# Optimization experiments

Hardware: AMD Instinct MI355X
Metric: run time of the kernel (lower is better)

Reference implementation:

```python
import jax, jax.numpy as jnp
import numpy as np

N = 16384      # points
C = 512        # channels (d_model)
D_INNER = 1024 # expand=2
D_STATE = 16
D_CONV = 4
DT_RANK = 32   # ceil(C/16)
MLP = 1024     # mlp_ratio=2
EPS = 1e-5


def setup_inputs() -> dict:
    key = jax.random.key(0)
    ks = jax.random.split(key, 16)
    s = 0.02
    feat = jax.random.normal(ks[0], (N, C), jnp.float32)
    perm = np.random.RandomState(0).permutation(N)
    order = jnp.asarray(perm, jnp.int32)
    inverse = jnp.asarray(np.argsort(perm), jnp.int32)
    inp = dict(
        feat=feat, order=order, inverse=inverse,
        ln1_w=jnp.ones((C,)), ln1_b=jnp.zeros((C,)),
        in_proj_w=s * jax.random.normal(ks[1], (2 * D_INNER, C)),
        conv_w=s * jax.random.normal(ks[2], (D_INNER, D_CONV)),
        conv_b=jnp.zeros((D_INNER,)),
        x_proj_w=s * jax.random.normal(ks[3], (DT_RANK + 2 * D_STATE, D_INNER)),
        dt_proj_w=s * jax.random.normal(ks[4], (D_INNER, DT_RANK)),
        dt_proj_b=jnp.full((D_INNER,), -2.0),  # softplus(-2) ~ small dt, like mamba init
        A_log=jnp.log(jnp.tile(jnp.arange(1, D_STATE + 1, dtype=jnp.float32)[None, :], (D_INNER, 1))),
        D_skip=jnp.ones((D_INNER,)),
        out_proj_w=s * jax.random.normal(ks[5], (C, D_INNER)),
        ln2_w=jnp.ones((C,)), ln2_b=jnp.zeros((C,)),
        ffn_w1=s * jax.random.normal(ks[6], (C, MLP)), ffn_b1=jnp.zeros((MLP,)),
        ffn_w2=s * jax.random.normal(ks[7], (MLP, C)), ffn_b2=jnp.zeros((C,)),
    )
    return inp


def _layer_norm(x, w, b):
    mu = jnp.mean(x, axis=-1, keepdims=True)
    var = jnp.mean(jnp.square(x - mu), axis=-1, keepdims=True)
    return (x - mu) * jax.lax.rsqrt(var + EPS) * w + b


def _mamba(x, in_proj_w, conv_w, conv_b, x_proj_w, dt_proj_w, dt_proj_b,
           A_log, D_skip, out_proj_w):
    # x: (L, C)
    L = x.shape[0]
    xz = x @ in_proj_w.T                      # (L, 2*D_INNER)
    xm, z = jnp.split(xz, 2, axis=-1)
    # depthwise causal conv1d, kernel D_CONV
    xp = jnp.pad(xm, ((D_CONV - 1, 0), (0, 0)))
    xc = conv_b + sum(xp[k:k + L] * conv_w[:, k] for k in range(D_CONV))
    xc = jax.nn.silu(xc)                      # (L, D_INNER)
    dbc = xc @ x_proj_w.T                     # (L, DT_RANK + 2*D_STATE)
    dt, Bm, Cm = jnp.split(dbc, [DT_RANK, DT_RANK + D_STATE], axis=-1)
    dt = jax.nn.softplus(dt @ dt_proj_w.T + dt_proj_b)  # (L, D_INNER)
    A = -jnp.exp(A_log)                       # (D_INNER, D_STATE)

    def step(h, inp):
        dt_t, B_t, C_t, x_t = inp             # (D_INNER,), (D_STATE,), (D_STATE,), (D_INNER,)
        dA = jnp.exp(dt_t[:, None] * A)       # (D_INNER, D_STATE)
        h = dA * h + (dt_t * x_t)[:, None] * B_t[None, :]
        return h, h @ C_t                     # y_t: (D_INNER,)

    h0 = jnp.zeros((D_INNER, D_STATE), xm.dtype)
    _, ys = jax.lax.scan(step, h0, (dt, Bm, Cm, xc))
    y = (ys + xc * D_skip) * jax.nn.silu(z)
    return y @ out_proj_w.T                   # (L, C)


def reference(feat, order, inverse, ln1_w, ln1_b, in_proj_w, conv_w, conv_b,
              x_proj_w, dt_proj_w, dt_proj_b, A_log, D_skip, out_proj_w,
              ln2_w, ln2_b, ffn_w1, ffn_b1, ffn_w2, ffn_b2):
    f = feat[order]                           # gather by serialized order
    x = f + _mamba(_layer_norm(f, ln1_w, ln1_b), in_proj_w, conv_w, conv_b,
                   x_proj_w, dt_proj_w, dt_proj_b, A_log, D_skip, out_proj_w)
    h = _layer_norm(x, ln2_w, ln2_b)
    x = x + (jax.nn.gelu(h @ ffn_w1 + ffn_b1, approximate=False) @ ffn_w2 + ffn_b2)
    return x[inverse]                         # scatter back to original order
```

## Files before the change

kernel.cpp:

```cpp
#include <hip/hip_runtime.h>


#define DEV __device__ __forceinline__

typedef unsigned short u16;
typedef u16    u16x8  __attribute__((ext_vector_type(8)));
typedef __bf16 bf16x8 __attribute__((ext_vector_type(8)));
typedef float  f32x4  __attribute__((ext_vector_type(4)));

static constexpr int L_SEQ = 16384;
static constexpr int LC    = 64;
static constexpr int NCH   = 256;

DEV u16 f2b(float x){
  union { float f; unsigned u; } c; c.f = x;
  unsigned u = c.u;
  return (u16)((u + 0x7fffu + ((u >> 16) & 1u)) >> 16);
}
DEV float b2f(u16 h){
  union { unsigned u; float f; } c; c.u = ((unsigned)h) << 16;
  return c.f;
}
DEV int ldix(const void* p, int l, bool is64){
  return is64 ? (int)((const long long*)p)[l] : ((const int*)p)[l];
}
DEV float siluf(float x){ return x / (1.f + __expf(-x)); }
DEV float softplusf(float x){ return x > 20.f ? x : log1pf(__expf(x)); }
DEV float geluf(float x){ return 0.5f * x * (1.f + erff(x * 0.70710678118f)); }

DEV void gld_lds16(const u16* g, u16* l){
  __builtin_amdgcn_global_load_lds(
      (const __attribute__((address_space(1))) unsigned*)g,
      (__attribute__((address_space(3))) unsigned*)l, 16, 0, 0);
}

DEV void pow16(float r, float* a){
  float r2 = r * r, r4 = r2 * r2, r8 = r4 * r4;
  a[0] = r;        a[1] = r2;       a[2] = r2 * r;    a[3] = r4;
  a[4] = r4 * r;   a[5] = r4 * r2;  a[6] = r4 * a[2]; a[7] = r8;
  a[8] = r8 * r;   a[9] = r8 * r2;  a[10] = r8 * a[2]; a[11] = r8 * r4;
  a[12] = r8 * a[4]; a[13] = r8 * a[5]; a[14] = r8 * a[6]; a[15] = r8 * r8;
}

__global__ __launch_bounds__(256) void fill_k(float* out, float v, unsigned n){
  unsigned i = blockIdx.x * 256 + threadIdx.x;
  if (i < n) out[i] = v;
}

__global__ void detect_k(const int* ord32, int* flag){
  flag[0] = (ord32[1] == 0 && ord32[3] == 0 && ord32[5] == 0) ? 1 : 0;
  flag[1] = 0;
}

__global__ __launch_bounds__(256) void checkA_k(const float* __restrict__ alog,
                                                int* flag){
  int i = blockIdx.x * 256 + threadIdx.x;
  int s = i & 15;
  float v = alog[i];
  float base = alog[i - s];
  if (fabsf(v - (base + __logf((float)(s + 1)))) > 1e-4f) atomicOr(flag + 1, 1);
}

struct NT4 { const float* src[4]; unsigned off[5]; };
__global__ __launch_bounds__(256) void normw_k(NT4 t, u16* dst){
  unsigned i = blockIdx.x * 256 + threadIdx.x;
  if (i >= t.off[4]) return;
  int s = 0;
  #pragma unroll
  for (int k = 1; k <= 3; k++) s += (i >= t.off[k]) ? 1 : 0;
  dst[i] = f2b(t.src[s][i - t.off[s]]);
}

__global__ __launch_bounds__(256) void convT_kernel(const float* __restrict__ in,
                                                    u16* __restrict__ out, int K, int N){
  __shared__ float t[32][33];
  int k0 = blockIdx.x * 32, n0 = blockIdx.y * 32;
  int tx = threadIdx.x & 31, ty = threadIdx.x >> 5;
  #pragma unroll
  for (int i = 0; i < 32; i += 8)
    t[ty + i][tx] = in[(size_t)(k0 + ty + i) * N + n0 + tx];
  __syncthreads();
  #pragma unroll
  for (int i = 0; i < 32; i += 8)
    out[(size_t)(n0 + ty + i) * K + k0 + tx] = f2b(t[tx][ty + i]);
}

__global__ __launch_bounds__(256) void gather_ln1(const float* __restrict__ feat,
    const void* order, const float* __restrict__ w, const float* __restrict__ b,
    const int* flag, u16* __restrict__ x1b){
  __shared__ float rs_[256], rq_[256];
  const bool is64 = flag[0] != 0;
  int l = blockIdx.x, tid = threadIdx.x;
  int src = ldix(order, l, is64);
  float v0 = feat[(size_t)src * 512 + tid];
  float v1 = feat[(size_t)src * 512 + tid + 256];
  rs_[tid] = v0 + v1; rq_[tid] = v0 * v0 + v1 * v1;
  __syncthreads();
  for (int o = 128; o; o >>= 1){
    if (tid < o){ rs_[tid] += rs_[tid + o]; rq_[tid] += rq_[tid + o]; }
    __syncthreads();
  }
  float mu = rs_[0] * (1.f / 512.f);
  float var = rq_[0] * (1.f / 512.f) - mu * mu;
  float rstd = rsqrtf(var + 1e-5f);
  x1b[(size_t)l * 512 + tid]       = f2b((v0 - mu) * rstd * w[tid]       + b[tid]);
  x1b[(size_t)l * 512 + tid + 256] = f2b((v1 - mu) * rstd * w[tid + 256] + b[tid + 256]);
}

__global__ __launch_bounds__(256) void ln2_kernel(const float* __restrict__ x,
    const float* __restrict__ w, const float* __restrict__ b, u16* __restrict__ h2b){
  __shared__ float rs_[256], rq_[256];
  int l = blockIdx.x, tid = threadIdx.x;
  float v0 = x[(size_t)l * 512 + tid];
  float v1 = x[(size_t)l * 512 + tid + 256];
  rs_[tid] = v0 + v1; rq_[tid] = v0 * v0 + v1 * v1;
  __syncthreads();
  for (int o = 128; o; o >>= 1){
    if (tid < o){ rs_[tid] += rs_[tid + o]; rq_[tid] += rq_[tid + o]; }
    __syncthreads();
  }
  float mu = rs_[0] * (1.f / 512.f);
  float var = rq_[0] * (1.f / 512.f) - mu * mu;
  float rstd = rsqrtf(var + 1e-5f);
  h2b[(size_t)l * 512 + tid]       = f2b((v0 - mu) * rstd * w[tid]       + b[tid]);
  h2b[(size_t)l * 512 + tid + 256] = f2b((v1 - mu) * rstd * w[tid + 256] + b[tid + 256]);
}

__global__ __launch_bounds__(256) void conv_silu(const u16* __restrict__ xm,
    const float* __restrict__ cw, const float* __restrict__ cb, u16* __restrict__ xcb){
  constexpr int TT = 8;
  const int tid = threadIdx.x;
  const int d0 = (tid & 127) * 8;
  const int t0 = (blockIdx.x * 2 + (tid >> 7)) * TT;

  float wk[4][8], bias[8];
  #pragma unroll
  for (int j = 0; j < 8; j++) bias[j] = cb[d0 + j];
  #pragma unroll
  for (int j = 0; j < 8; j++){
    f32x4 v = *(const f32x4*)(cw + (d0 + j) * 4);
    wk[0][j] = v[0]; wk[1][j] = v[1]; wk[2][j] = v[2]; wk[3][j] = v[3];
  }

  float win[3][8];
  #pragma unroll
  for (int k = 0; k < 3; k++){
    int tt = t0 - 3 + k;
    if (tt >= 0){
      u16x8 v = *(const u16x8*)(xm + (size_t)tt * 1024 + d0);
      #pragma unroll
      for (int j = 0; j < 8; j++) win[k][j] = b2f(v[j]);
    } else {
      #pragma unroll
      for (int j = 0; j < 8; j++) win[k][j] = 0.f;
    }
  }

  #pragma unroll
  for (int t = 0; t < TT; t++){
    u16x8 v = *(const u16x8*)(xm + (size_t)(t0 + t) * 1024 + d0);
    u16x8 o;
    float cu[8];
    #pragma unroll
    for (int j = 0; j < 8; j++){
      cu[j] = b2f(v[j]);
      float acc = bias[j] + win[0][j] * wk[0][j] + win[1][j] * wk[1][j]
                + win[2][j] * wk[2][j] + cu[j] * wk[3][j];
      o[j] = f2b(siluf(acc));
    }
    *(u16x8*)(xcb + (size_t)(t0 + t) * 1024 + d0) = o;
    #pragma unroll
    for (int j = 0; j < 8; j++){
      win[0][j] = win[1][j]; win[1][j] = win[2][j]; win[2][j] = cu[j];
    }
  }
}

enum { M_BF16 = 0, M_INPROJ = 1, M_DT = 2, M_RES = 3, M_GELU = 4, M_FFN2 = 5 };

template<int MODE>
DEV void gemm_epilogue(float v, int m, int n, int N,
    float* __restrict__ outf, u16* __restrict__ outb, u16* __restrict__ outb2,
    const float* __restrict__ auxf, const float* __restrict__ auxw,
    const void* ordv, bool is64){
  size_t o = (size_t)m * N + n;
  if constexpr (MODE == M_BF16){
    outb[o] = f2b(v);
  } else if constexpr (MODE == M_INPROJ){
    if (n < 1024) outb [(size_t)m * 1024 + n]          = f2b(v);
    else          outb2[(size_t)m * 1024 + (n - 1024)] = f2b(siluf(v));
  } else if constexpr (MODE == M_DT){
    outb[o] = f2b(softplusf(v + auxw[n]));
  } else if constexpr (MODE == M_RES){
    int src = ldix(ordv, m, is64);
    outf[o] = v + auxw[(size_t)src * 512 + n];
  } else if constexpr (MODE == M_GELU){
    outb[o] = f2b(geluf(v + auxw[n]));
  } else {
    outf[o] = v + auxw[n] + auxf[o];
  }
}

template<int BM, int BN, int WM, int WN, int MODE>
__global__ __launch_bounds__(256) void gemm_bt64(
    const u16* __restrict__ A, const u16* __restrict__ B,
    int N, int K, int lda, int ldb,
    float* __restrict__ outf, u16* __restrict__ outb, u16* __restrict__ outb2,
    const float* __restrict__ auxf, const float* __restrict__ auxw,
    const void* ordv, const int* flag){
  constexpr int BK = 64;
  constexpr int MI = WM / 16, NI = WN / 16;
  constexpr int WCOLS = BN / WN;
  constexpr int NA = BM * BK / (256 * 8);
  constexpr int NB = BN * BK / (256 * 8);
  __shared__ __align__(16) u16 sA[2][BM * BK];
  __shared__ __align__(16) u16 sB[2][BN * BK];
  const int tid  = threadIdx.x;
  const int wave = tid >> 6, lane = tid & 63;
  const int wr = wave / WCOLS, wc = wave % WCOLS;
  const int m0 = blockIdx.x * BM, n0 = blockIdx.y * BN;
  const int rr = lane & 15;
  const int qh = lane >> 4;

  f32x4 acc[MI][NI] = {};

  auto stage = [&](int buf, int k0){
    #pragma unroll
    for (int i = 0; i < NA; i++){
      int idx = tid + i * 256;
      int row = idx >> 3, sub = idx & 7;
      int cg = sub ^ (row & 7);
      gld_lds16(A + (size_t)(m0 + row) * lda + k0 + cg * 8, &sA[buf][idx * 8]);
    }
    #pragma unroll
    for (int i = 0; i < NB; i++){
      int idx = tid + i * 256;
      int row = idx >> 3, sub = idx & 7;
      int cg = sub ^ (row & 7);
      gld_lds16(B + (size_t)(n0 + row) * ldb + k0 + cg * 8, &sB[buf][idx * 8]);
    }
  };

  stage(0, 0);
  const int nst = K / BK;
  for (int st = 0; st < nst; st++){
    const int cur = st & 1;
    __syncthreads();
    if (st + 1 < nst) stage(cur ^ 1, (st + 1) * BK);
    #pragma unroll
    for (int kk = 0; kk < 2; kk++){
      bf16x8 af[MI], bfr[NI];
      #pragma unroll
      for (int i = 0; i < MI; i++){
        int R = wr * WM + i * 16 + rr;
        int sub = (kk * 4 + qh) ^ (R & 7);
        af[i] = *(const bf16x8*)(&sA[cur][R * BK + sub * 8]);
      }
      #pragma unroll
      for (int j = 0; j < NI; j++){
        int R = wc * WN + j * 16 + rr;
        int sub = (kk * 4 + qh) ^ (R & 7);
        bfr[j] = *(const bf16x8*)(&sB[cur][R * BK + sub * 8]);
      }
      #pragma unroll
      for (int i = 0; i < MI; i++)
        #pragma unroll
        for (int j = 0; j < NI; j++)
          acc[i][j] = __builtin_amdgcn_mfma_f32_16x16x32_bf16(af[i], bfr[j], acc[i][j], 0, 0, 0);
    }
  }

  const bool is64 = flag ? (flag[0] != 0) : false;
  #pragma unroll
  for (int i = 0; i < MI; i++)
    #pragma unroll
    for (int j = 0; j < NI; j++)
      #pragma unroll
      for (int r = 0; r < 4; r++){
        int m = m0 + wr * WM + i * 16 + ((lane >> 4) << 2) + r;
        int n = n0 + wc * WN + j * 16 + (lane & 15);
        gemm_epilogue<MODE>(acc[i][j][r], m, n, N, outf, outb, outb2,
                            auxf, auxw, ordv, is64);
      }
}

template<int BM, int BN, int WM, int WN, int MODE>
__global__ __launch_bounds__(256) void gemm_bt(
    const u16* __restrict__ A, const u16* __restrict__ B,
    int N, int K, int lda, int ldb,
    float* __restrict__ outf, u16* __restrict__ outb, u16* __restrict__ outb2,
    const float* __restrict__ auxf, const float* __restrict__ auxw,
    const void* ordv, const int* flag){
  constexpr int BK = 32;
  constexpr int MI = WM / 16, NI = WN / 16;
  constexpr int WCOLS = BN / WN;
  constexpr int NA = BM * 4 / 256;
  constexpr int NB = BN * 4 / 256;
  __shared__ __align__(16) u16 sA[BM * BK];
  __shared__ __align__(16) u16 sB[BN * BK];
  const int tid  = threadIdx.x;
  const int wave = tid >> 6, lane = tid & 63;
  const int wr = wave / WCOLS, wc = wave % WCOLS;
  const int m0 = blockIdx.x * BM, n0 = blockIdx.y * BN;
  const int rr = lane & 15;
  const int qk = (lane >> 4) * 8;

  f32x4 acc[MI][NI] = {};

  for (int k0 = 0; k0 < K; k0 += BK){
    #pragma unroll
    for (int i = 0; i < NA; i++){
      int idx = tid + i * 256;
      int r = idx >> 2, c = (idx & 3) * 8;
      gld_lds16(A + (size_t)(m0 + r) * lda + k0 + c, sA + (size_t)idx * 8);
    }
    #pragma unroll
    for (int i = 0; i < NB; i++){
      int idx = tid + i * 256;
      int r = idx >> 2, c = (idx & 3) * 8;
      gld_lds16(B + (size_t)(n0 + r) * ldb + k0 + c, sB + (size_t)idx * 8);
    }
    __syncthreads();

    bf16x8 af[MI], bfr[NI];
    #pragma unroll
    for (int i = 0; i < MI; i++)
      af[i] = *(const bf16x8*)(sA + (wr * WM + i * 16 + rr) * BK + qk);
    #pragma unroll
    for (int j = 0; j < NI; j++)
      bfr[j] = *(const bf16x8*)(sB + (wc * WN + j * 16 + rr) * BK + qk);
    #pragma unroll
    for (int i = 0; i < MI; i++)
      #pragma unroll
      for (int j = 0; j < NI; j++)
        acc[i][j] = __builtin_amdgcn_mfma_f32_16x16x32_bf16(af[i], bfr[j], acc[i][j], 0, 0, 0);
    __syncthreads();
  }

  const bool is64 = flag ? (flag[0] != 0) : false;
  #pragma unroll
  for (int i = 0; i < MI; i++)
    #pragma unroll
    for (int j = 0; j < NI; j++)
      #pragma unroll
      for (int r = 0; r < 4; r++){
        int m = m0 + wr * WM + i * 16 + ((lane >> 4) << 2) + r;
        int n = n0 + wc * WN + j * 16 + (lane & 15);
        gemm_epilogue<MODE>(acc[i][j][r], m, n, N, outf, outb, outb2,
                            auxf, auxw, ordv, is64);
      }
}

__global__ __launch_bounds__(256) void scan_pass1(const u16* __restrict__ dt,
    const u16* __restrict__ xc, const u16* __restrict__ dbc,
    const float* __restrict__ alog, const int* __restrict__ flag,
    u16* __restrict__ chP, u16* __restrict__ chH){
  __shared__ float sB[LC * 16];
  const int chunk = blockIdx.x;
  const int d = blockIdx.y * 256 + threadIdx.x;
  const int t0 = chunk * LC;
  for (int i = threadIdx.x; i < LC * 16; i += 256){
    int t = i >> 4, s = i & 15;
    sB[i] = b2f(dbc[(size_t)(t0 + t) * 64 + 32 + s]);
  }
  __syncthreads();
  float h[16];
  #pragma unroll
  for (int s = 0; s < 16; s++) h[s] = 0.f;
  float P[16];
  const bool fastA = (flag[1] == 0);
  if (fastA){
    const float a0 = -__expf(alog[(size_t)d * 16]);
    float R = 1.f;
    for (int t = 0; t < LC; t++){
      float dtv = b2f(dt[(size_t)(t0 + t) * 1024 + d]);
      float xv  = b2f(xc[(size_t)(t0 + t) * 1024 + d]);
      float dtx = dtv * xv;
      float r = __expf(dtv * a0);
      R *= r;
      float a_[16];
      pow16(r, a_);
      #pragma unroll
      for (int s = 0; s < 16; s++)
        h[s] = a_[s] * h[s] + dtx * sB[t * 16 + s];
    }
    pow16(R, P);
  } else {
    float A[16];
    #pragma unroll
    for (int s = 0; s < 16; s++){
      A[s] = -__expf(alog[(size_t)d * 16 + s]);
      P[s] = 1.f;
    }
    for (int t = 0; t < LC; t++){
      float dtv = b2f(dt[(size_t)(t0 + t) * 1024 + d]);
      float xv  = b2f(xc[(size_t)(t0 + t) * 1024 + d]);
      float dtx = dtv * xv;
      #pragma unroll
      for (int s = 0; s < 16; s++){
        float a = __expf(dtv * A[s]);
        P[s] *= a;
        h[s] = a * h[s] + dtx * sB[t * 16 + s];
      }
    }
  }
  #pragma unroll
  for (int s = 0; s < 16; s++){
    chP[((size_t)chunk * 16 + s) * 1024 + d] = f2b(P[s]);
    chH[((size_t)chunk * 16 + s) * 1024 + d] = f2b(h[s]);
  }
}

__global__ __launch_bounds__(64) void carry_scan(const u16* chP, const u16* chH,
                                                 u16* hin){
  int id = blockIdx.x * 64 + threadIdx.x;
  float h = 0.f;
  for (int k = 0; k < NCH; k += 8){
    float P[8], E[8];
    #pragma unroll
    for (int j = 0; j < 8; j++){
      P[j] = b2f(chP[(size_t)(k + j) * 16384 + id]);
      E[j] = b2f(chH[(size_t)(k + j) * 16384 + id]);
    }
    #pragma unroll
    for (int j = 0; j < 8; j++){
      hin[(size_t)(k + j) * 16384 + id] = f2b(h);
      h = P[j] * h + E[j];
    }
  }
}

__global__ __launch_bounds__(256) void scan_pass3(const u16* __restrict__ dt,
    const u16* xc, const u16* __restrict__ dbc,
    const float* __restrict__ alog, const int* __restrict__ flag,
    const u16* __restrict__ hin,
    const float* __restrict__ dskip, const u16* __restrict__ zsil, u16* yb){
  __shared__ float sBC[LC * 32];
  const int chunk = blockIdx.x;
  const int d = blockIdx.y * 256 + threadIdx.x;
  const int t0 = chunk * LC;
  for (int i = threadIdx.x; i < LC * 32; i += 256){
    int t = i >> 5, c = i & 31;
    sBC[i] = b2f(dbc[(size_t)(t0 + t) * 64 + 32 + c]);
  }
  __syncthreads();
  float h[16];
  #pragma unroll
  for (int s = 0; s < 16; s++)
    h[s] = b2f(hin[((size_t)chunk * 16 + s) * 1024 + d]);
  const float Dv = dskip[d];
  const bool fastA = (flag[1] == 0);
  if (fastA){
    const float a0 = -__expf(alog[(size_t)d * 16]);
    for (int t = 0; t < LC; t++){
      float dtv = b2f(dt[(size_t)(t0 + t) * 1024 + d]);
      float xv  = b2f(xc[(size_t)(t0 + t) * 1024 + d]);
      float dtx = dtv * xv;
      float r = __expf(dtv * a0);
      float a_[16];
      pow16(r, a_);
      float y = 0.f;
      #pragma unroll
      for (int s = 0; s < 16; s++){
        h[s] = a_[s] * h[s] + dtx * sBC[t * 32 + s];
        y += h[s] * sBC[t * 32 + 16 + s];
      }
      float rv = (y + xv * Dv) * b2f(zsil[(size_t)(t0 + t) * 1024 + d]);
      yb[(size_t)(t0 + t) * 1024 + d] = f2b(rv);
    }
  } else {
    float A[16];
    #pragma unroll
    for (int s = 0; s < 16; s++) A[s] = -__expf(alog[(size_t)d * 16 + s]);
    for (int t = 0; t < LC; t++){
      float dtv = b2f(dt[(size_t)(t0 + t) * 1024 + d]);
      float xv  = b2f(xc[(size_t)(t0 + t) * 1024 + d]);
      float dtx = dtv * xv;
      float y = 0.f;
      #pragma unroll
      for (int s = 0; s < 16; s++){
        float a = __expf(dtv * A[s]);
        h[s] = a * h[s] + dtx * sBC[t * 32 + s];
        y += h[s] * sBC[t * 32 + 16 + s];
      }
      float rv = (y + xv * Dv) * b2f(zsil[(size_t)(t0 + t) * 1024 + d]);
      yb[(size_t)(t0 + t) * 1024 + d] = f2b(rv);
    }
  }
}

__global__ __launch_bounds__(256) void final_gather(const float* __restrict__ xfin,
    const void* inv, const int* flag, float* __restrict__ out){
  const bool is64 = flag[0] != 0;
  int i = blockIdx.x, tid = threadIdx.x;
  int src = ldix(inv, i, is64);
  out[(size_t)i * 512 + tid]       = xfin[(size_t)src * 512 + tid];
  out[(size_t)i * 512 + tid + 256] = xfin[(size_t)src * 512 + tid + 256];
}

extern "C" void kernel_launch(void* const* d_in, const int* in_sizes, int n_in,
                              void* d_out, int out_size, void* d_ws, size_t ws_size,
                              hipStream_t stream){
  float* out = (float*)d_out;
  char* w = (char*)d_ws;

  constexpr size_t OFF_W1T  = 3342336;
  constexpr size_t OFF_W2T  = OFF_W1T + 1048576;
  constexpr size_t OFF_FLAG = OFF_W2T + 1048576;
  constexpr size_t OFF_XMB  = 5439744;
  constexpr size_t OFF_ZSIL = OFF_XMB  + 33554432;
  constexpr size_t OFF_XCB  = OFF_ZSIL + 33554432;
  constexpr size_t OFF_X1B  = OFF_XCB  + 33554432;
  constexpr size_t OFF_DBC  = OFF_X1B  + 16777216;
  constexpr size_t OFF_CHP  = OFF_X1B;
  constexpr size_t OFF_CHH  = OFF_X1B  + 8388608;
  constexpr size_t WS_NEED  = OFF_DBC  + 2097152;

  int code = 0;
  static const int want[20] = {8388608,16384,16384,512,512,1048576,4096,1024,
                               65536,32768,1024,16384,1024,524288,512,512,
                               524288,1024,524288,512};
  if (n_in != 20) code = 1000;
  else {
    for (int i = 0; i < 20 && !code; i++)
      if (in_sizes[i] != want[i]) code = 2000 + i * 50;
    if (!code && out_size != 8388608) code = 3000;
    if (!code && ws_size < WS_NEED)   code = 4000;
  }
  if (code){
    unsigned n = (unsigned)(out_size > 0 ? out_size : 1);
    fill_k<<<(n + 255) / 256, 256, 0, stream>>>(out, (float)code, n);
    return;
  }

  u16*   w1tb = (u16*)(w + OFF_W1T);
  u16*   w2tb = (u16*)(w + OFF_W2T);
  int*   flag = (int*)(w + OFF_FLAG);
  u16*   xmb  = (u16*)(w + OFF_XMB);
  u16*   zsil = (u16*)(w + OFF_ZSIL);
  u16*   xcb  = (u16*)(w + OFF_XCB);
  u16*   x1b  = (u16*)(w + OFF_X1B);
  u16*   dbcb = (u16*)(w + OFF_DBC);
  u16*   chP  = (u16*)(w + OFF_CHP);
  u16*   chH  = (u16*)(w + OFF_CHH);
  float* x    = (float*)(w + OFF_XMB);
  float* xfin = (float*)(w + OFF_XCB);
  u16* dtb  = xmb;
  u16* yb   = xcb;
  u16* midb = zsil;
  u16* h2b  = x1b;
  u16* hin  = chP;

  u16* nb = (u16*)w;
  u16* inpjn  = nb;
  u16* xpjn   = nb + 1048576;
  u16* dtpjn  = nb + 1114112;
  u16* outpjn = nb + 1146880;
  NT4 t;
  t.src[0] = (const float*)d_in[5];  t.src[1] = (const float*)d_in[8];
  t.src[2] = (const float*)d_in[9];  t.src[3] = (const float*)d_in[13];
  t.off[0] = 0; t.off[1] = 1048576; t.off[2] = 1114112; t.off[3] = 1146880; t.off[4] = 1671168;

  detect_k<<<1, 1, 0, stream>>>((const int*)d_in[1], flag);
  checkA_k<<<64, 256, 0, stream>>>((const float*)d_in[11], flag);
  normw_k<<<(1671168 + 255) / 256, 256, 0, stream>>>(t, nb);
  convT_kernel<<<dim3(16, 32), 256, 0, stream>>>((const float*)d_in[16], w1tb, 512, 1024);
  convT_kernel<<<dim3(32, 16), 256, 0, stream>>>((const float*)d_in[18], w2tb, 1024, 512);

  gather_ln1<<<L_SEQ, 256, 0, stream>>>((const float*)d_in[0], d_in[1],
      (const float*)d_in[3], (const float*)d_in[4], flag, x1b);

  gemm_bt64<128,128,64,64,M_INPROJ><<<dim3(128,16),256,0,stream>>>(
      x1b, inpjn, 2048, 512, 512, 512, nullptr, xmb, zsil, nullptr, nullptr, nullptr, nullptr);

  conv_silu<<<1024, 256, 0, stream>>>(xmb,
      (const float*)d_in[6], (const float*)d_in[7], xcb);

  gemm_bt64<64,64,16,64,M_BF16><<<dim3(256,1),256,0,stream>>>(
      xcb, xpjn, 64, 1024, 1024, 1024, nullptr, dbcb, nullptr, nullptr, nullptr, nullptr, nullptr);

  gemm_bt<128,128,64,64,M_DT><<<dim3(128,8),256,0,stream>>>(
      dbcb, dtpjn, 1024, 32, 64, 32, nullptr, dtb, nullptr, nullptr,
      (const float*)d_in[10], nullptr, nullptr);

  scan_pass1<<<dim3(NCH,4),256,0,stream>>>(dtb, xcb, dbcb,
      (const float*)d_in[11], flag, chP, chH);
  carry_scan<<<256,64,0,stream>>>(chP, chH, hin);
  scan_pass3<<<dim3(NCH,4),256,0,stream>>>(dtb, xcb, dbcb,
      (const float*)d_in[11], flag, hin, (const float*)d_in[12], zsil, yb);

  gemm_bt64<128,128,64,64,M_RES><<<dim3(128,4),256,0,stream>>>(
      yb, outpjn, 512, 1024, 1024, 1024, x, nullptr, nullptr, nullptr,
      (const float*)d_in[0], d_in[1], flag);

  ln2_kernel<<<L_SEQ,256,0,stream>>>(x, (const float*)d_in[14], (const float*)d_in[15], h2b);

  gemm_bt64<128,128,64,64,M_GELU><<<dim3(128,8),256,0,stream>>>(
      h2b, w1tb, 1024, 512, 512, 512, nullptr, midb, nullptr, nullptr,
      (const float*)d_in[17], nullptr, nullptr);

  gemm_bt64<128,128,64,64,M_FFN2><<<dim3(128,4),256,0,stream>>>(
      midb, w2tb, 512, 1024, 1024, 1024, xfin, nullptr, nullptr, x,
      (const float*)d_in[19], nullptr, nullptr);

  final_gather<<<L_SEQ,256,0,stream>>>(xfin, d_in[2], flag, out);
}
```

Before: 528.1 us.

## Triple-buffer GEMM with BK=32, explicit vmcnt waits and XCD-aware block remap

Replaces the double-buffered BK=64 GEMM with a three-stage pipeline over BK=32 tiles. It prefetches two stages ahead and uses explicit s_waitcnt vmcnt counts plus raw barriers in place of __syncthreads, so global-to-LDS loads overlap MFMA work more deeply. Block IDs are also remapped in groups of 8, likely to match the XCD dispatch pattern for better L2 locality. The cost is two barriers per smaller k-step and hardcoded vmcnt literals that are only correct if the compiler emits exactly the expected number of loads per stage.

```diff
diff --git a/kernel.cpp b/kernel.cpp
--- a/kernel.cpp
+++ b/kernel.cpp
@@ -202,25 +202,30 @@
 }
 
 template<int BM, int BN, int WM, int WN, int MODE>
-__global__ __launch_bounds__(256) void gemm_bt64(
+__global__ __launch_bounds__(256) void gemm_p2(
     const u16* __restrict__ A, const u16* __restrict__ B,
     int N, int K, int lda, int ldb,
     float* __restrict__ outf, u16* __restrict__ outb, u16* __restrict__ outb2,
     const float* __restrict__ auxf, const float* __restrict__ auxw,
     const void* ordv, const int* flag){
-  constexpr int BK = 64;
+  constexpr int BK = 32;
   constexpr int MI = WM / 16, NI = WN / 16;
   constexpr int WCOLS = BN / WN;
   constexpr int NA = BM * BK / (256 * 8);
   constexpr int NB = BN * BK / (256 * 8);
-  __shared__ __align__(16) u16 sA[2][BM * BK];
-  __shared__ __align__(16) u16 sB[2][BN * BK];
+  constexpr int LPS = NA + NB;
+  static_assert(LPS == 2 || LPS == 4, "vmcnt literals assume LPS in {2,4}");
+  __shared__ __align__(16) u16 sA[3][BM * BK];
+  __shared__ __align__(16) u16 sB[3][BN * BK];
   const int tid  = threadIdx.x;
   const int wave = tid >> 6, lane = tid & 63;
   const int wr = wave / WCOLS, wc = wave % WCOLS;
-  const int m0 = blockIdx.x * BM, n0 = blockIdx.y * BN;
+  const int nwg = gridDim.x * gridDim.y;
+  int bid = blockIdx.y * gridDim.x + blockIdx.x;
+  bid = (bid & 7) * (nwg >> 3) + (bid >> 3);
+  const int m0 = (bid % gridDim.x) * BM, n0 = (bid / gridDim.x) * BN;
   const int rr = lane & 15;
-  const int qh = lane >> 4;
+  const int qc = lane >> 4;
 
   f32x4 acc[MI][NI] = {};
 
@@ -228,46 +233,60 @@
     #pragma unroll
     for (int i = 0; i < NA; i++){
       int idx = tid + i * 256;
-      int row = idx >> 3, sub = idx & 7;
-      int cg = sub ^ (row & 7);
+      int row = idx >> 2, sub = idx & 3;
+      int cg = sub ^ (row & 3);
       gld_lds16(A + (size_t)(m0 + row) * lda + k0 + cg * 8, &sA[buf][idx * 8]);
     }
     #pragma unroll
     for (int i = 0; i < NB; i++){
       int idx = tid + i * 256;
-      int row = idx >> 3, sub = idx & 7;
-      int cg = sub ^ (row & 7);
+      int row = idx >> 2, sub = idx & 3;
+      int cg = sub ^ (row & 3);
       gld_lds16(B + (size_t)(n0 + row) * ldb + k0 + cg * 8, &sB[buf][idx * 8]);
     }
   };
 
+  const int nst = K / BK;
   stage(0, 0);
-  const int nst = K / BK;
+  if (nst > 1) stage(1, BK);
   for (int st = 0; st < nst; st++){
-    const int cur = st & 1;
-    __syncthreads();
-    if (st + 1 < nst) stage(cur ^ 1, (st + 1) * BK);
-    #pragma unroll
-    for (int kk = 0; kk < 2; kk++){
-      bf16x8 af[MI], bfr[NI];
-      #pragma unroll
-      for (int i = 0; i < MI; i++){
-        int R = wr * WM + i * 16 + rr;
-        int sub = (kk * 4 + qh) ^ (R & 7);
-        af[i] = *(const bf16x8*)(&sA[cur][R * BK + sub * 8]);
-      }
-      #pragma unroll
-      for (int j = 0; j < NI; j++){
-        int R = wc * WN + j * 16 + rr;
-        int sub = (kk * 4 + qh) ^ (R & 7);
-        bfr[j] = *(const bf16x8*)(&sB[cur][R * BK + sub * 8]);
-      }
-      #pragma unroll
-      for (int i = 0; i < MI; i++)
-        #pragma unroll
-        for (int j = 0; j < NI; j++)
-          acc[i][j] = __builtin_amdgcn_mfma_f32_16x16x32_bf16(af[i], bfr[j], acc[i][j], 0, 0, 0);
-    }
+    if (st + 2 < nst) stage((st + 2) % 3, (st + 2) * BK);
+    const int nf = (st + 2 < nst) ? 2 : ((st + 1 < nst) ? 1 : 0);
+    if (nf == 2){
+      if constexpr (LPS == 4) asm volatile("s_waitcnt vmcnt(8)" ::: "memory");
+      else                    asm volatile("s_waitcnt vmcnt(4)" ::: "memory");
+    } else if (nf == 1){
+      if constexpr (LPS == 4) asm volatile("s_waitcnt vmcnt(4)" ::: "memory");
+      else                    asm volatile("s_waitcnt vmcnt(2)" ::: "memory");
+    } else {
+      asm volatile("s_waitcnt vmcnt(0)" ::: "memory");
+    }
+    __builtin_amdgcn_s_barrier();
+    __builtin_amdgcn_sched_barrier(0);
+
+    const int cur = st % 3;
+    bf16x8 af[MI], bfr[NI];
+    #pragma unroll
+    for (int i = 0; i < MI; i++){
+      int R = wr * WM + i * 16 + rr;
+      int slot = qc ^ (R & 3);
+      af[i] = *(const bf16x8*)(&sA[cur][R * BK + slot * 8]);
+    }
+    #pragma unroll
+    for (int j = 0; j < NI; j++){
+      int R = wc * WN + j * 16 + rr;
+      int slot = qc ^ (R & 3);
+      bfr[j] = *(const bf16x8*)(&sB[cur][R * BK + slot * 8]);
+    }
+    #pragma unroll
+    for (int i = 0; i < MI; i++)
+      #pragma unroll
+      for (int j = 0; j < NI; j++)
+        acc[i][j] = __builtin_amdgcn_mfma_f32_16x16x32_bf16(af[i], bfr[j], acc[i][j], 0, 0, 0);
+
+    asm volatile("s_waitcnt lgkmcnt(0)" ::: "memory");
+    __builtin_amdgcn_s_barrier();
+    __builtin_amdgcn_sched_barrier(0);
   }
 
   const bool is64 = flag ? (flag[0] != 0) : false;
@@ -570,13 +589,13 @@
   gather_ln1<<<L_SEQ, 256, 0, stream>>>((const float*)d_in[0], d_in[1],
       (const float*)d_in[3], (const float*)d_in[4], flag, x1b);
 
-  gemm_bt64<128,128,64,64,M_INPROJ><<<dim3(128,16),256,0,stream>>>(
+  gemm_p2<128,128,64,64,M_INPROJ><<<dim3(128,16),256,0,stream>>>(
       x1b, inpjn, 2048, 512, 512, 512, nullptr, xmb, zsil, nullptr, nullptr, nullptr, nullptr);
 
   conv_silu<<<1024, 256, 0, stream>>>(xmb,
       (const float*)d_in[6], (const float*)d_in[7], xcb);
 
-  gemm_bt64<64,64,16,64,M_BF16><<<dim3(256,1),256,0,stream>>>(
+  gemm_p2<64,64,16,64,M_BF16><<<dim3(256,1),256,0,stream>>>(
       xcb, xpjn, 64, 1024, 1024, 1024, nullptr, dbcb, nullptr, nullptr, nullptr, nullptr, nullptr);
 
   gemm_bt<128,128,64,64,M_DT><<<dim3(128,8),256,0,stream>>>(
@@ -589,17 +608,17 @@
   scan_pass3<<<dim3(NCH,4),256,0,stream>>>(dtb, xcb, dbcb,
       (const float*)d_in[11], flag, hin, (const float*)d_in[12], zsil, yb);
 
-  gemm_bt64<128,128,64,64,M_RES><<<dim3(128,4),256,0,stream>>>(
+  gemm_p2<128,128,64,64,M_RES><<<dim3(128,4),256,0,stream>>>(
       yb, outpjn, 512, 1024, 1024, 1024, x, nullptr, nullptr, nullptr,
       (const float*)d_in[0], d_in[1], flag);
 
   ln2_kernel<<<L_SEQ,256,0,stream>>>(x, (const float*)d_in[14], (const float*)d_in[15], h2b);
 
-  gemm_bt64<128,128,64,64,M_GELU><<<dim3(128,8),256,0,stream>>>(
+  gemm_p2<128,128,64,64,M_GELU><<<dim3(128,8),256,0,stream>>>(
       h2b, w1tb, 1024, 512, 512, 512, nullptr, midb, nullptr, nullptr,
       (const float*)d_in[17], nullptr, nullptr);
 
-  gemm_bt64<128,128,64,64,M_FFN2><<<dim3(128,4),256,0,stream>>>(
+  gemm_p2<128,128,64,64,M_FFN2><<<dim3(128,4),256,0,stream>>>(
       midb, w2tb, 512, 1024, 1024, 1024, xfin, nullptr, nullptr, x,
       (const float*)d_in[19], nullptr, nullptr);
 
```

After: 572.1 us. 8.3% more time.
